# Kernel optimization log

Hardware: AMD Instinct MI355X
Metric: run time of the kernel (lower is better)

## Reference

```python
import jax, jax.numpy as jnp
import numpy as np

LN_EPS = 1e-5  # torch LayerNorm default
EPS = 1e-8     # slot-attention eps

def _ln(x, g, b):
    m = jnp.mean(x, axis=-1, keepdims=True)
    v = jnp.mean(jnp.square(x - m), axis=-1, keepdims=True)
    return (x - m) * jax.lax.rsqrt(v + LN_EPS) * g + b

def setup_inputs() -> dict:
    key = jax.random.key(0)
    ks = jax.random.split(key, 16)
    b, d, n_s, h = 131072, 256, 16, 256
    w_scale = d ** -0.5
    return {
        "inputs": jax.random.normal(ks[0], (b, 1, d), jnp.float32),
        "noise": jax.random.normal(ks[1], (n_s, d), jnp.float32),
        "slots_mu": jax.random.normal(ks[2], (1, d), jnp.float32),
        "slots_sigma": jax.random.uniform(ks[3], (1, d), jnp.float32),
        "Wq": jax.random.normal(ks[4], (d, d), jnp.float32) * w_scale,
        "bq": jnp.zeros((d,), jnp.float32),
        "Wk": jax.random.normal(ks[5], (d, d), jnp.float32) * w_scale,
        "bk": jnp.zeros((d,), jnp.float32),
        "Wv": jax.random.normal(ks[6], (d, d), jnp.float32) * w_scale,
        "bv": jnp.zeros((d,), jnp.float32),
        "W_ih": jax.random.normal(ks[7], (3 * d, d), jnp.float32) * w_scale,
        "W_hh": jax.random.normal(ks[8], (3 * d, d), jnp.float32) * w_scale,
        "b_ih": jnp.zeros((3 * d,), jnp.float32),
        "b_hh": jnp.zeros((3 * d,), jnp.float32),
        "W1": jax.random.normal(ks[9], (h, d), jnp.float32) * w_scale,
        "b1": jnp.zeros((h,), jnp.float32),
        "W2": jax.random.normal(ks[10], (d, h), jnp.float32) * (h ** -0.5),
        "b2": jnp.zeros((d,), jnp.float32),
        "g_in": jnp.ones((d,), jnp.float32),
        "be_in": jnp.zeros((d,), jnp.float32),
        "g_s": jnp.ones((d,), jnp.float32),
        "be_s": jnp.zeros((d,), jnp.float32),
        "g_f": jnp.ones((d,), jnp.float32),
        "be_f": jnp.zeros((d,), jnp.float32),
    }

def reference(inputs, noise, slots_mu, slots_sigma, Wq, bq, Wk, bk, Wv, bv,
              W_ih, W_hh, b_ih, b_hh, W1, b1, W2, b2,
              g_in, be_in, g_s, be_s, g_f, be_f):
    b, w, d = inputs.shape  # w == 1 required by the module's LayerNorm(dim)
    x = inputs.reshape(b, w * d)
    scale = d ** -0.5
    iters = 3

    slots = slots_mu + slots_sigma * noise  # (n_s, d), reparameterized normal

    x = _ln(x, g_in, be_in)
    k = x @ Wk.T + bk  # (b, d)
    v = x @ Wv.T + bv  # (b, d)

    for _ in range(iters):
        slots_prev = slots
        s = _ln(slots, g_s, be_s)
        q = s @ Wq.T + bq                      # (n_s, d)
        dots = jnp.einsum('nd,bd->nb', q, k) * scale
        attn = jax.nn.softmax(dots, axis=0) + EPS   # softmax over slots
        attn = attn / jnp.sum(attn, axis=-1, keepdims=True)
        updates = jnp.einsum('bd,nb->nd', v, attn)  # (n_s, d)
        # torch GRUCell
        gx = updates @ W_ih.T + b_ih                # (n_s, 3d)
        gh = slots_prev @ W_hh.T + b_hh
        xr, xz, xn = jnp.split(gx, 3, axis=-1)
        hr, hz, hn = jnp.split(gh, 3, axis=-1)
        r = jax.nn.sigmoid(xr + hr)
        z = jax.nn.sigmoid(xz + hz)
        n = jnp.tanh(xn + r * hn)
        slots = (1.0 - z) * n + z * slots_prev
        ff = jax.nn.relu(_ln(slots, g_f, be_f) @ W1.T + b1) @ W2.T + b2
        slots = slots + ff
    return slots
```

## Files before the change

kernel.cpp:

```cpp
#include <hip/hip_runtime.h>
#include <stdint.h>

#define B_ROWS 131072
#define SCALE 0.0625f
#define LN_EPS 1e-5f
#define ATTN_EPS 1e-8f

#define BIG_BLOCKS 512
#define BIG_THREADS 512
#define ROWS_PER_BLOCK (B_ROWS / BIG_BLOCKS)
#define ROWS_PER_WAVE  (ROWS_PER_BLOCK / 8)
#define NSLICE 8

#define WS_PARTU 0
#define WS_PARTS (WS_PARTU + 512*4096)
#define WS_U     (WS_PARTS + 512*16)
#define WS_S     (WS_U + 4096)
#define WS_SLOTS (WS_S + 64)
#define WS_MID   (WS_SLOTS + 4096)
#define WS_GX    (WS_MID + 4096)
#define WS_GH    (WS_GX + 12288)
#define WS_H1    (WS_GH + 12288)
#define WS_QKG   (WS_H1 + 4096)
#define WS_QB    (WS_QKG + 4096)
#define WS_WIHV  (WS_QB + 64)
#define WS_BGX   (WS_WIHV + 196608)
#define WS_WQKG  (WS_BGX + 768)
#define WS_U2G   (WS_WQKG + 65536)
#define WS_U1    (WS_U2G + 256)
#define WS_C1    (WS_U1 + 256)

__device__ __forceinline__ float dot16(const float* __restrict__ w, const float* s)
{
  float4 w0 = *(const float4*)(w);
  float4 w1 = *(const float4*)(w + 4);
  float4 w2 = *(const float4*)(w + 8);
  float4 w3 = *(const float4*)(w + 12);
  float4 s0 = *(const float4*)(s);
  float4 s1 = *(const float4*)(s + 4);
  float4 s2 = *(const float4*)(s + 8);
  float4 s3 = *(const float4*)(s + 12);
  float a = 0.f;
  a = fmaf(w0.x, s0.x, a); a = fmaf(w0.y, s0.y, a);
  a = fmaf(w0.z, s0.z, a); a = fmaf(w0.w, s0.w, a);
  a = fmaf(w1.x, s1.x, a); a = fmaf(w1.y, s1.y, a);
  a = fmaf(w1.z, s1.z, a); a = fmaf(w1.w, s1.w, a);
  a = fmaf(w2.x, s2.x, a); a = fmaf(w2.y, s2.y, a);
  a = fmaf(w2.z, s2.z, a); a = fmaf(w2.w, s2.w, a);
  a = fmaf(w3.x, s3.x, a); a = fmaf(w3.y, s3.y, a);
  a = fmaf(w3.z, s3.z, a); a = fmaf(w3.w, s3.w, a);
  return a;
}

__global__ __launch_bounds__(256) void k_pre1(
    const float* __restrict__ Wq, const float* __restrict__ bq,
    const float* __restrict__ Wk, const float* __restrict__ bk,
    const float* __restrict__ Wv, const float* __restrict__ bv,
    const float* __restrict__ W_ih, const float* __restrict__ b_ih,
    const float* __restrict__ g_in, const float* __restrict__ be_in,
    float* __restrict__ ws)
{
  int bid = blockIdx.x, t = threadIdx.x;
  int wave = t >> 6, lane = t & 63;
  if (bid < 32) {
#pragma unroll
    for (int q = 0; q < 4; q++)
      ws[WS_PARTU + bid * 1024 + q * 256 + t] = 0.f;
  } else if (bid == 256) {
    if (t < 128) ws[WS_PARTS + t] = 0.f;
  }
  if (bid < 192) {
    __shared__ __align__(16) float sW[4 * 256];
    __shared__ __align__(16) float sBv[256];
    int j0 = bid * 4;
#pragma unroll
    for (int r = 0; r < 4; r++) sW[r * 256 + t] = W_ih[(j0 + r) * 256 + t];
    sBv[t] = bv[t];
    __syncthreads();
    int d = t;
    float a0 = 0.f, a1 = 0.f, a2 = 0.f, a3 = 0.f;
#pragma unroll 8
    for (int dd = 0; dd < 256; dd++) {
      float v = Wv[dd * 256 + d];
      a0 = fmaf(sW[0 * 256 + dd], v, a0);
      a1 = fmaf(sW[1 * 256 + dd], v, a1);
      a2 = fmaf(sW[2 * 256 + dd], v, a2);
      a3 = fmaf(sW[3 * 256 + dd], v, a3);
    }
    ws[WS_WIHV + (j0 + 0) * 256 + d] = a0;
    ws[WS_WIHV + (j0 + 1) * 256 + d] = a1;
    ws[WS_WIHV + (j0 + 2) * 256 + d] = a2;
    ws[WS_WIHV + (j0 + 3) * 256 + d] = a3;
    float s = 0.f;
#pragma unroll
    for (int q = 0; q < 4; q++) {
      int idx = lane * 4 + q;
      s = fmaf(sW[wave * 256 + idx], sBv[idx], s);
    }
#pragma unroll
    for (int m = 1; m <= 32; m <<= 1) s += __shfl_xor(s, m);
    if (lane == 0) ws[WS_BGX + j0 + wave] = b_ih[j0 + wave] + s;
  } else if (bid < 256) {
    __shared__ __align__(16) float sKc[4 * 256];
    __shared__ __align__(16) float sBq[256];
    int c0 = (bid - 192) * 4;
#pragma unroll
    for (int r = 0; r < 4; r++) sKc[r * 256 + t] = Wk[t * 256 + c0 + r];
    sBq[t] = bq[t];
    __syncthreads();
    int d = t;
    float a0 = 0.f, a1 = 0.f, a2 = 0.f, a3 = 0.f;
#pragma unroll 8
    for (int i = 0; i < 256; i++) {
      float wq = Wq[i * 256 + d];
      a0 = fmaf(wq, sKc[0 * 256 + i], a0);
      a1 = fmaf(wq, sKc[1 * 256 + i], a1);
      a2 = fmaf(wq, sKc[2 * 256 + i], a2);
      a3 = fmaf(wq, sKc[3 * 256 + i], a3);
    }
    ws[WS_WQKG + (c0 + 0) * 256 + d] = SCALE * g_in[c0 + 0] * a0;
    ws[WS_WQKG + (c0 + 1) * 256 + d] = SCALE * g_in[c0 + 1] * a1;
    ws[WS_WQKG + (c0 + 2) * 256 + d] = SCALE * g_in[c0 + 2] * a2;
    ws[WS_WQKG + (c0 + 3) * 256 + d] = SCALE * g_in[c0 + 3] * a3;
    float s = 0.f;
#pragma unroll
    for (int q = 0; q < 4; q++) {
      int idx = lane * 4 + q;
      s = fmaf(sBq[idx], sKc[wave * 256 + idx], s);
    }
#pragma unroll
    for (int m = 1; m <= 32; m <<= 1) s += __shfl_xor(s, m);
    if (lane == 0) ws[WS_U2G + c0 + wave] = SCALE * g_in[c0 + wave] * s;
  } else {
    __shared__ __align__(16) float sBe[256];
    __shared__ __align__(16) float sT2[256];
    sBe[t] = be_in[t];
    __syncthreads();
    float a = 0.f;
#pragma unroll 8
    for (int dp = 0; dp < 256; dp += 4) {
      float4 w = *(const float4*)(Wk + t * 256 + dp);
      a = fmaf(w.x, sBe[dp], fmaf(w.y, sBe[dp + 1],
          fmaf(w.z, sBe[dp + 2], fmaf(w.w, sBe[dp + 3], a))));
    }
    sT2[t] = a + bk[t];
    __syncthreads();
    float u = 0.f;
#pragma unroll 8
    for (int i = 0; i < 256; i++)
      u = fmaf(Wq[i * 256 + t], sT2[i], u);
    ws[WS_U1 + t] = u;
    if (wave == 0) {
      float s = 0.f;
#pragma unroll
      for (int q = 0; q < 4; q++) {
        int idx = lane * 4 + q;
        s = fmaf(bq[idx], sT2[idx], s);
      }
#pragma unroll
      for (int m = 1; m <= 32; m <<= 1) s += __shfl_xor(s, m);
      if (lane == 0) ws[WS_C1] = s;
    }
  }
}

__global__ __launch_bounds__(256) void k_qkg(
    const float* __restrict__ noise, const float* __restrict__ mu,
    const float* __restrict__ sigma, const float* __restrict__ g_s,
    const float* __restrict__ be_s, float* __restrict__ ws, int init)
{
  __shared__ __align__(16) float sS[16 * 260];
  __shared__ __align__(16) float sAux[512];
  __shared__ __align__(16) float sStat[32];
  int bid = blockIdx.x, t = threadIdx.x;
  for (int n = 0; n < 16; n++) {
    float v;
    if (init) v = fmaf(sigma[t], noise[n * 256 + t], mu[t]);
    else      v = ws[WS_SLOTS + n * 256 + t];
    sS[n * 260 + t] = v;
    if (init && bid == 0) ws[WS_SLOTS + n * 256 + t] = v;
  }
  __syncthreads();
  { int n = t >> 4, c = t & 15;
    float s1 = 0.f, s2 = 0.f;
    for (int k = 0; k < 16; k++) {
      float x = sS[n * 260 + c * 16 + k];
      s1 += x; s2 = fmaf(x, x, s2);
    }
    sAux[n * 16 + c] = s1; sAux[256 + n * 16 + c] = s2; }
  __syncthreads();
  if (t < 16) {
    float s1 = 0.f, s2 = 0.f;
    for (int c = 0; c < 16; c++) { s1 += sAux[t * 16 + c]; s2 += sAux[256 + t * 16 + c]; }
    float m = s1 * (1.f / 256.f);
    float v = fmaxf(fmaf(-m, m, s2 * (1.f / 256.f)), 0.f);
    sStat[t] = m; sStat[16 + t] = rsqrtf(v + LN_EPS);
  }
  __syncthreads();
  { float gs = g_s[t], bs = be_s[t];
    for (int n = 0; n < 16; n++) {
      float m = sStat[n], rs = sStat[16 + n];
      sS[n * 260 + t] = fmaf((sS[n * 260 + t] - m) * rs, gs, bs);
    } }
  __syncthreads();
  if (bid < 64) {
    int cr = t >> 6, n = (t >> 2) & 15, ks = t & 3;
    int c = bid * 4 + cr;
    const float* wrow = ws + WS_WQKG + c * 256 + ks * 64;
    const float* srow = &sS[n * 260 + ks * 64];
    float acc = 0.f;
#pragma unroll
    for (int i = 0; i < 16; i++) {
      float4 w = *(const float4*)(wrow + i * 4);
      float4 s4 = *(const float4*)(srow + i * 4);
      acc = fmaf(w.x, s4.x, fmaf(w.y, s4.y, fmaf(w.z, s4.z, fmaf(w.w, s4.w, acc))));
    }
    sAux[t] = acc;
    __syncthreads();
    if (t < 64) {
      int cr2 = t >> 4, n2 = t & 15;
      int c2 = bid * 4 + cr2;
      int b = cr2 * 64 + n2 * 4;
      float s = sAux[b] + sAux[b + 1] + sAux[b + 2] + sAux[b + 3];
      ws[WS_QKG + n2 * 256 + c2] = s + ws[WS_U2G + c2];
    }
  } else {
    int n = t >> 4, ks = t & 15;
    float acc = 0.f;
    for (int k = 0; k < 16; k++)
      acc = fmaf(sS[n * 260 + ks * 16 + k], ws[WS_U1 + ks * 16 + k], acc);
    sAux[t] = acc;
    __syncthreads();
    if (t < 16) {
      float s = 0.f;
      for (int k = 0; k < 16; k++) s += sAux[t * 16 + k];
      ws[WS_QB + t] = SCALE * (s + ws[WS_C1]);
    }
  }
}

__global__ __launch_bounds__(512, 2) void k_big(
    const float* __restrict__ X, float* __restrict__ ws)
{
  __shared__ __align__(16) float red[4 * 4096];
  __shared__ __align__(16) float redS[128];
  int t = threadIdx.x;
  int wave = t >> 6, lane = t & 63;
  int p = lane >> 4, g = lane & 15;

  const float* qkg = ws + WS_QKG;
  float qw[4][16];
  float qs[4];
#pragma unroll
  for (int i = 0; i < 4; i++) {
    const float* rp = qkg + (4 * p + i) * 256 + g * 16;
#pragma unroll
    for (int jq = 0; jq < 4; jq++) {
      float4 v4 = *(const float4*)(rp + 4 * jq);
      qw[i][4 * jq + 0] = v4.x; qw[i][4 * jq + 1] = v4.y;
      qw[i][4 * jq + 2] = v4.z; qw[i][4 * jq + 3] = v4.w;
    }
    float s = 0.f;
#pragma unroll
    for (int j = 0; j < 16; j++) s += qw[i][j];
    qs[i] = s;
  }
#pragma unroll
  for (int m = 1; m <= 8; m <<= 1) {
#pragma unroll
    for (int i = 0; i < 4; i++) qs[i] += __shfl_xor(qs[i], m);
  }
  float qb0[4];
  {
    float4 q4 = *(const float4*)(ws + WS_QB + 4 * p);
    qb0[0] = q4.x; qb0[1] = q4.y; qb0[2] = q4.z; qb0[3] = q4.w;
  }

  float P[4][16];
#pragma unroll
  for (int i = 0; i < 4; i++)
#pragma unroll
    for (int j = 0; j < 16; j++) P[i][j] = 0.f;
  float Q[4] = {0.f, 0.f, 0.f, 0.f};
  float Sa[4] = {0.f, 0.f, 0.f, 0.f};

  size_t rowbase = (size_t)blockIdx.x * ROWS_PER_BLOCK + (size_t)wave * ROWS_PER_WAVE;
  const float* base = X + rowbase * 256 + g * 16;

  float4 cA0 = *(const float4*)(base + 0);
  float4 cB0 = *(const float4*)(base + 4);
  float4 cC0 = *(const float4*)(base + 8);
  float4 cD0 = *(const float4*)(base + 12);
  float4 cA1 = *(const float4*)(base + 256);
  float4 cB1 = *(const float4*)(base + 260);
  float4 cC1 = *(const float4*)(base + 264);
  float4 cD1 = *(const float4*)(base + 268);

#pragma unroll 1
  for (int r = 0; r < ROWS_PER_WAVE; r += 2) {
    const float* nx = base + (size_t)((r + 2 < ROWS_PER_WAVE) ? (r + 2) : 0) * 256;
    float4 pA0 = *(const float4*)(nx + 0);
    float4 pB0 = *(const float4*)(nx + 4);
    float4 pC0 = *(const float4*)(nx + 8);
    float4 pD0 = *(const float4*)(nx + 12);
    float4 pA1 = *(const float4*)(nx + 256);
    float4 pB1 = *(const float4*)(nx + 260);
    float4 pC1 = *(const float4*)(nx + 264);
    float4 pD1 = *(const float4*)(nx + 268);

    float x0[16], x1[16];
    x0[0] = cA0.x; x0[1] = cA0.y; x0[2] = cA0.z; x0[3] = cA0.w;
    x0[4] = cB0.x; x0[5] = cB0.y; x0[6] = cB0.z; x0[7] = cB0.w;
    x0[8] = cC0.x; x0[9] = cC0.y; x0[10] = cC0.z; x0[11] = cC0.w;
    x0[12] = cD0.x; x0[13] = cD0.y; x0[14] = cD0.z; x0[15] = cD0.w;
    x1[0] = cA1.x; x1[1] = cA1.y; x1[2] = cA1.z; x1[3] = cA1.w;
    x1[4] = cB1.x; x1[5] = cB1.y; x1[6] = cB1.z; x1[7] = cB1.w;
    x1[8] = cC1.x; x1[9] = cC1.y; x1[10] = cC1.z; x1[11] = cC1.w;
    x1[12] = cD1.x; x1[13] = cD1.y; x1[14] = cD1.z; x1[15] = cD1.w;

    float s10 = 0.f, s20 = 0.f, s11 = 0.f, s21 = 0.f;
    float d0[4] = {0.f, 0.f, 0.f, 0.f};
    float d1[4] = {0.f, 0.f, 0.f, 0.f};
#pragma unroll
    for (int j = 0; j < 16; j++) {
      s10 += x0[j]; s20 = fmaf(x0[j], x0[j], s20);
      s11 += x1[j]; s21 = fmaf(x1[j], x1[j], s21);
#pragma unroll
      for (int i = 0; i < 4; i++) {
        d0[i] = fmaf(qw[i][j], x0[j], d0[i]);
        d1[i] = fmaf(qw[i][j], x1[j], d1[i]);
      }
    }
#pragma unroll
    for (int m = 1; m <= 8; m <<= 1) {
      s10 += __shfl_xor(s10, m); s11 += __shfl_xor(s11, m);
      s20 += __shfl_xor(s20, m); s21 += __shfl_xor(s21, m);
#pragma unroll
      for (int i = 0; i < 4; i++) {
        d0[i] += __shfl_xor(d0[i], m);
        d1[i] += __shfl_xor(d1[i], m);
      }
    }
    float mean0 = s10 * (1.f / 256.f), mean1 = s11 * (1.f / 256.f);
    float var0 = fmaxf(fmaf(-mean0, mean0, s20 * (1.f / 256.f)), 0.f);
    float var1 = fmaxf(fmaf(-mean1, mean1, s21 * (1.f / 256.f)), 0.f);
    float rs0 = rsqrtf(var0 + LN_EPS), rs1 = rsqrtf(var1 + LN_EPS);
    float mrs0 = mean0 * rs0, mrs1 = mean1 * rs1;

    float dsc0[4], dsc1[4];
#pragma unroll
    for (int i = 0; i < 4; i++) {
      dsc0[i] = fmaf(rs0, d0[i], fmaf(-mrs0, qs[i], qb0[i]));
      dsc1[i] = fmaf(rs1, d1[i], fmaf(-mrs1, qs[i], qb0[i]));
    }

    float mx0 = fmaxf(fmaxf(dsc0[0], dsc0[1]), fmaxf(dsc0[2], dsc0[3]));
    float mx1 = fmaxf(fmaxf(dsc1[0], dsc1[1]), fmaxf(dsc1[2], dsc1[3]));
    mx0 = fmaxf(mx0, __shfl_xor(mx0, 16)); mx1 = fmaxf(mx1, __shfl_xor(mx1, 16));
    mx0 = fmaxf(mx0, __shfl_xor(mx0, 32)); mx1 = fmaxf(mx1, __shfl_xor(mx1, 32));
    float e0[4], e1[4];
#pragma unroll
    for (int i = 0; i < 4; i++) {
      e0[i] = __expf(dsc0[i] - mx0);
      e1[i] = __expf(dsc1[i] - mx1);
    }
    float se0 = e0[0] + e0[1] + e0[2] + e0[3];
    float se1 = e1[0] + e1[1] + e1[2] + e1[3];
    se0 += __shfl_xor(se0, 16); se1 += __shfl_xor(se1, 16);
    se0 += __shfl_xor(se0, 32); se1 += __shfl_xor(se1, 32);
    float inv0 = 1.0f / se0, inv1 = 1.0f / se1;
    float a0v[4], ar0[4], a1v[4], ar1[4];
#pragma unroll
    for (int i = 0; i < 4; i++) {
      a0v[i] = fmaf(e0[i], inv0, ATTN_EPS); ar0[i] = a0v[i] * rs0;
      a1v[i] = fmaf(e1[i], inv1, ATTN_EPS); ar1[i] = a1v[i] * rs1;
    }

#pragma unroll
    for (int j = 0; j < 16; j++) {
#pragma unroll
      for (int i = 0; i < 4; i++) {
        P[i][j] = fmaf(ar0[i], x0[j], P[i][j]);
        P[i][j] = fmaf(ar1[i], x1[j], P[i][j]);
      }
    }
#pragma unroll
    for (int i = 0; i < 4; i++) {
      Q[i] = fmaf(a0v[i], mrs0, Q[i]);
      Q[i] = fmaf(a1v[i], mrs1, Q[i]);
      Sa[i] += a0v[i];
      Sa[i] += a1v[i];
    }

    cA0 = pA0; cB0 = pB0; cC0 = pC0; cD0 = pD0;
    cA1 = pA1; cB1 = pB1; cC1 = pC1; cD1 = pD1;
  }

  int slot = wave & 3;
  if (wave < 4) {
#pragma unroll
    for (int i = 0; i < 4; i++) {
#pragma unroll
      for (int jq = 0; jq < 4; jq++) {
        float4 v4;
        v4.x = P[i][4 * jq + 0] - Q[i]; v4.y = P[i][4 * jq + 1] - Q[i];
        v4.z = P[i][4 * jq + 2] - Q[i]; v4.w = P[i][4 * jq + 3] - Q[i];
        *(float4*)&red[slot * 4096 + (4 * p + i) * 256 + g * 16 + jq * 4] = v4;
      }
    }
  }
  if (g == 0) {
#pragma unroll
    for (int i = 0; i < 4; i++) redS[wave * 16 + 4 * p + i] = Sa[i];
  }
  __syncthreads();
  if (wave >= 4) {
#pragma unroll
    for (int i = 0; i < 4; i++) {
#pragma unroll
      for (int jq = 0; jq < 4; jq++) {
        float4* dst = (float4*)&red[slot * 4096 + (4 * p + i) * 256 + g * 16 + jq * 4];
        float4 c = *dst;
        c.x += P[i][4 * jq + 0] - Q[i]; c.y += P[i][4 * jq + 1] - Q[i];
        c.z += P[i][4 * jq + 2] - Q[i]; c.w += P[i][4 * jq + 3] - Q[i];
        *dst = c;
      }
    }
  }
  __syncthreads();
  int slice = blockIdx.x & 7;
#pragma unroll
  for (int k = 0; k < 8; k++) {
    int idx = k * 512 + t;
    float v = red[idx] + red[4096 + idx] + red[8192 + idx] + red[12288 + idx];
    atomicAdd(&ws[WS_PARTU + (size_t)slice * 4096 + idx], v);
  }
  if (t < 16) {
    float sv = 0.f;
#pragma unroll
    for (int w = 0; w < 8; w++) sv += redS[w * 16 + t];
    atomicAdd(&ws[WS_PARTS + slice * 16 + t], sv);
  }
}

__global__ __launch_bounds__(256) void k_gxgh(
    const float* __restrict__ W_hh, const float* __restrict__ b_hh,
    const float* __restrict__ g_in, const float* __restrict__ be_in,
    float* __restrict__ ws)
{
  __shared__ __align__(16) float sU[16 * 260];
  __shared__ __align__(16) float sInv[16];
  int bid = blockIdx.x, t = threadIdx.x;
  bool isgx = bid < 64;
  if (isgx && t < 16) {
    float s = 0.f;
#pragma unroll
    for (int sl = 0; sl < NSLICE; sl++) s += ws[WS_PARTS + sl * 16 + t];
    sInv[t] = 1.0f / s;
  }
  __syncthreads();
  if (isgx) {
    float gi = g_in[t], bi = be_in[t];
    for (int n = 0; n < 16; n++) {
      float acc = 0.f;
#pragma unroll
      for (int sl = 0; sl < NSLICE; sl++)
        acc += ws[WS_PARTU + (size_t)sl * 4096 + n * 256 + t];
      sU[n * 260 + t] = fmaf(gi * acc, sInv[n], bi);
    }
  } else {
    for (int n = 0; n < 16; n++)
      sU[n * 260 + t] = ws[WS_SLOTS + n * 256 + t];
  }
  __syncthreads();
  int jr = t >> 4, n = t & 15;
  if (jr < 12) {
    int j = (isgx ? bid : bid - 64) * 12 + jr;
    const float* srow = &sU[n * 260];
    const float* wrow = isgx ? (ws + WS_WIHV + j * 256) : (W_hh + j * 256);
    float acc = isgx ? ws[WS_BGX + j] : b_hh[j];
#pragma unroll 8
    for (int k = 0; k < 64; k++) {
      float4 w = *(const float4*)(wrow + k * 4);
      float4 s4 = *(const float4*)(srow + k * 4);
      acc = fmaf(w.x, s4.x, fmaf(w.y, s4.y, fmaf(w.z, s4.z, fmaf(w.w, s4.w, acc))));
    }
    if (isgx) ws[WS_GX + n * 768 + j] = acc;
    else      ws[WS_GH + n * 768 + j] = acc;
  }
}

__global__ __launch_bounds__(512) void k_tail(
    const float* __restrict__ W1, const float* __restrict__ b1,
    const float* __restrict__ g_f, const float* __restrict__ be_f,
    const float* __restrict__ W2, const float* __restrict__ b2v,
    const float* __restrict__ g_s, const float* __restrict__ be_s,
    float* __restrict__ out, float* __restrict__ ws, int last)
{
  __shared__ __align__(16) float sMid[256];
  __shared__ __align__(16) float sVec[256];
  __shared__ __align__(16) float sH1[256];
  __shared__ __align__(16) float sNew[256];
  __shared__ __align__(16) float sR[32];
  int n = blockIdx.x, t = threadIdx.x;
  int wv = t >> 6, lane = t & 63;
  int j16 = t >> 4, kt = t & 15;

  {
    int gid = n * 512 + t;
    float4 z4 = {0.f, 0.f, 0.f, 0.f};
    *(float4*)&ws[WS_PARTU + gid * 4] = z4;
    if (n == 0 && t < 128) ws[WS_PARTS + t] = 0.f;
  }

  float mid = 0.f;
  if (t < 256) {
    float xr = ws[WS_GX + n * 768 + t],       hr = ws[WS_GH + n * 768 + t];
    float xz = ws[WS_GX + n * 768 + 256 + t], hz = ws[WS_GH + n * 768 + 256 + t];
    float xn = ws[WS_GX + n * 768 + 512 + t], hn = ws[WS_GH + n * 768 + 512 + t];
    float sp = ws[WS_SLOTS + n * 256 + t];
    float r = 1.f / (1.f + __expf(-(xr + hr)));
    float z = 1.f / (1.f + __expf(-(xz + hz)));
    float nn = tanhf(fmaf(r, hn, xn));
    mid = fmaf(z, sp - nn, nn);
    sMid[t] = mid;
  }

  {
    float s1 = mid, s2 = mid * mid;
#pragma unroll
    for (int m = 1; m <= 32; m <<= 1) {
      s1 += __shfl_xor(s1, m); s2 += __shfl_xor(s2, m);
    }
    if (lane == 0) { sR[wv] = s1; sR[8 + wv] = s2; }
  }
  __syncthreads();
  {
    float s1 = sR[0] + sR[1] + sR[2] + sR[3] + sR[4] + sR[5] + sR[6] + sR[7];
    float s2 = sR[8] + sR[9] + sR[10] + sR[11] + sR[12] + sR[13] + sR[14] + sR[15];
    float mean = s1 * (1.f / 256.f);
    float var = fmaxf(fmaf(-mean, mean, s2 * (1.f / 256.f)), 0.f);
    float rs = rsqrtf(var + LN_EPS);
    if (t < 256)
      sVec[t] = fmaf((sMid[t] - mean) * rs, g_f[t], be_f[t]);
  }
  __syncthreads();

#pragma unroll 2
  for (int pass = 0; pass < 8; pass++) {
    int j = pass * 32 + j16;
    float a = dot16(W1 + (size_t)j * 256 + kt * 16, sVec + kt * 16);
    a += __shfl_xor(a, 1); a += __shfl_xor(a, 2);
    a += __shfl_xor(a, 4); a += __shfl_xor(a, 8);
    if (kt == 0) sH1[j] = fmaxf(a + b1[j], 0.f);
  }
  __syncthreads();

#pragma unroll 2
  for (int pass = 0; pass < 8; pass++) {
    int d = pass * 32 + j16;
    float a = dot16(W2 + (size_t)d * 256 + kt * 16, sH1 + kt * 16);
    a += __shfl_xor(a, 1); a += __shfl_xor(a, 2);
    a += __shfl_xor(a, 4); a += __shfl_xor(a, 8);
    if (kt == 0) sNew[d] = a + b2v[d] + sMid[d];
  }
  __syncthreads();
  if (t < 256) {
    float v = sNew[t];
    ws[WS_SLOTS + n * 256 + t] = v;
    out[n * 256 + t] = v;
  }
  if (last) return;

  {
    float v = (t < 256) ? sNew[t] : 0.f;
    float s1 = v, s2 = v * v;
#pragma unroll
    for (int m = 1; m <= 32; m <<= 1) {
      s1 += __shfl_xor(s1, m); s2 += __shfl_xor(s2, m);
    }
    if (lane == 0) { sR[wv] = s1; sR[8 + wv] = s2; }
  }
  __syncthreads();
  {
    float s1 = sR[0] + sR[1] + sR[2] + sR[3] + sR[4] + sR[5] + sR[6] + sR[7];
    float s2 = sR[8] + sR[9] + sR[10] + sR[11] + sR[12] + sR[13] + sR[14] + sR[15];
    float mean = s1 * (1.f / 256.f);
    float var = fmaxf(fmaf(-mean, mean, s2 * (1.f / 256.f)), 0.f);
    float rs = rsqrtf(var + LN_EPS);
    if (t < 256)
      sVec[t] = fmaf((sNew[t] - mean) * rs, g_s[t], be_s[t]);
  }
  __syncthreads();
#pragma unroll 2
  for (int pass = 0; pass < 8; pass++) {
    int c = pass * 32 + j16;
    float a = dot16(ws + WS_WQKG + (size_t)c * 256 + kt * 16, sVec + kt * 16);
    a += __shfl_xor(a, 1); a += __shfl_xor(a, 2);
    a += __shfl_xor(a, 4); a += __shfl_xor(a, 8);
    if (kt == 0) ws[WS_QKG + n * 256 + c] = a + ws[WS_U2G + c];
  }
  {
    float pq = (t < 256) ? sVec[t] * ws[WS_U1 + t] : 0.f;
#pragma unroll
    for (int m = 1; m <= 32; m <<= 1) pq += __shfl_xor(pq, m);
    if (lane == 0) sR[wv] = pq;
  }
  __syncthreads();
  if (t == 0) {
    float s = sR[0] + sR[1] + sR[2] + sR[3] + sR[4] + sR[5] + sR[6] + sR[7];
    ws[WS_QB + n] = SCALE * (s + ws[WS_C1]);
  }
}

extern "C" void kernel_launch(void* const* d_in, const int* in_sizes, int n_in,
                              void* d_out, int out_size, void* d_ws, size_t ws_size,
                              hipStream_t stream)
{
  (void)in_sizes; (void)n_in; (void)out_size; (void)ws_size;
  const float* inputs = (const float*)d_in[0];
  const float* noise  = (const float*)d_in[1];
  const float* mu     = (const float*)d_in[2];
  const float* sigma  = (const float*)d_in[3];
  const float* Wq     = (const float*)d_in[4];
  const float* bq     = (const float*)d_in[5];
  const float* Wk     = (const float*)d_in[6];
  const float* bk     = (const float*)d_in[7];
  const float* Wv     = (const float*)d_in[8];
  const float* bv     = (const float*)d_in[9];
  const float* W_ih   = (const float*)d_in[10];
  const float* W_hh   = (const float*)d_in[11];
  const float* b_ih   = (const float*)d_in[12];
  const float* b_hh   = (const float*)d_in[13];
  const float* W1     = (const float*)d_in[14];
  const float* b1     = (const float*)d_in[15];
  const float* W2     = (const float*)d_in[16];
  const float* b2     = (const float*)d_in[17];
  const float* g_in   = (const float*)d_in[18];
  const float* be_in  = (const float*)d_in[19];
  const float* g_s    = (const float*)d_in[20];
  const float* be_s   = (const float*)d_in[21];
  const float* g_f    = (const float*)d_in[22];
  const float* be_f   = (const float*)d_in[23];
  float* ws = (float*)d_ws;
  float* out = (float*)d_out;

  hipLaunchKernelGGL(k_pre1, dim3(257), dim3(256), 0, stream,
                     Wq, bq, Wk, bk, Wv, bv, W_ih, b_ih, g_in, be_in, ws);
  hipLaunchKernelGGL(k_qkg, dim3(65), dim3(256), 0, stream,
                     noise, mu, sigma, g_s, be_s, ws, 1);
  for (int it = 0; it < 3; it++) {
    hipLaunchKernelGGL(k_big, dim3(BIG_BLOCKS), dim3(BIG_THREADS), 0, stream,
                       inputs, ws);
    hipLaunchKernelGGL(k_gxgh, dim3(128), dim3(256), 0, stream,
                       W_hh, b_hh, g_in, be_in, ws);
    hipLaunchKernelGGL(k_tail, dim3(16), dim3(512), 0, stream,
                       W1, b1, g_f, be_f, W2, b2, g_s, be_s,
                       out, ws, (it == 2) ? 1 : 0);
  }
}
```

Before: 549.0 us.

## Fuse GRU gate and tail kernels via software grid barrier

Merges the gx/gh gate kernel and the slot tail kernel into one 128-block launch that uses an atomic-counter grid barrier, after which 16 blocks run the GRU/MLP tail with 256 threads instead of 512. This removes one kernel launch and its inter-kernel gap per iteration, which matters because the small kernels are latency-bound. The cost is a spin barrier that assumes all 128 blocks are co-resident, and half as many threads in the tail matvecs.

```diff
diff --git a/kernel.cpp b/kernel.cpp
--- a/kernel.cpp
+++ b/kernel.cpp
@@ -11,6 +11,7 @@
 #define ROWS_PER_BLOCK (B_ROWS / BIG_BLOCKS)
 #define ROWS_PER_WAVE  (ROWS_PER_BLOCK / 8)
 #define NSLICE 8
+#define SLOT_BLOCKS 128u
 
 #define WS_PARTU 0
 #define WS_PARTS (WS_PARTU + 512*4096)
@@ -29,6 +30,21 @@
 #define WS_U2G   (WS_WQKG + 65536)
 #define WS_U1    (WS_U2G + 256)
 #define WS_C1    (WS_U1 + 256)
+#define WS_CTR   (WS_C1 + 4)
+
+__device__ __forceinline__ void gridbar(unsigned int* ctr, unsigned int target)
+{
+  __syncthreads();
+  if (threadIdx.x == 0) {
+    __threadfence();
+    __hip_atomic_fetch_add(ctr, 1u, __ATOMIC_RELEASE, __HIP_MEMORY_SCOPE_AGENT);
+    while (__hip_atomic_load(ctr, __ATOMIC_RELAXED, __HIP_MEMORY_SCOPE_AGENT) < target) {
+      __builtin_amdgcn_s_sleep(1);
+    }
+    __threadfence();
+  }
+  __syncthreads();
+}
 
 __device__ __forceinline__ float dot16(const float* __restrict__ w, const float* s)
 {
@@ -68,6 +84,7 @@
       ws[WS_PARTU + bid * 1024 + q * 256 + t] = 0.f;
   } else if (bid == 256) {
     if (t < 128) ws[WS_PARTS + t] = 0.f;
+    if (t == 0) *((unsigned int*)(ws + WS_CTR)) = 0u;
   }
   if (bid < 192) {
     __shared__ __align__(16) float sW[4 * 256];
@@ -443,78 +460,81 @@
   }
 }
 
-__global__ __launch_bounds__(256) void k_gxgh(
+__global__ __launch_bounds__(256) void k_slot(
     const float* __restrict__ W_hh, const float* __restrict__ b_hh,
     const float* __restrict__ g_in, const float* __restrict__ be_in,
-    float* __restrict__ ws)
-{
-  __shared__ __align__(16) float sU[16 * 260];
-  __shared__ __align__(16) float sInv[16];
-  int bid = blockIdx.x, t = threadIdx.x;
-  bool isgx = bid < 64;
-  if (isgx && t < 16) {
-    float s = 0.f;
-#pragma unroll
-    for (int sl = 0; sl < NSLICE; sl++) s += ws[WS_PARTS + sl * 16 + t];
-    sInv[t] = 1.0f / s;
-  }
-  __syncthreads();
-  if (isgx) {
-    float gi = g_in[t], bi = be_in[t];
-    for (int n = 0; n < 16; n++) {
-      float acc = 0.f;
-#pragma unroll
-      for (int sl = 0; sl < NSLICE; sl++)
-        acc += ws[WS_PARTU + (size_t)sl * 4096 + n * 256 + t];
-      sU[n * 260 + t] = fmaf(gi * acc, sInv[n], bi);
-    }
-  } else {
-    for (int n = 0; n < 16; n++)
-      sU[n * 260 + t] = ws[WS_SLOTS + n * 256 + t];
-  }
-  __syncthreads();
-  int jr = t >> 4, n = t & 15;
-  if (jr < 12) {
-    int j = (isgx ? bid : bid - 64) * 12 + jr;
-    const float* srow = &sU[n * 260];
-    const float* wrow = isgx ? (ws + WS_WIHV + j * 256) : (W_hh + j * 256);
-    float acc = isgx ? ws[WS_BGX + j] : b_hh[j];
-#pragma unroll 8
-    for (int k = 0; k < 64; k++) {
-      float4 w = *(const float4*)(wrow + k * 4);
-      float4 s4 = *(const float4*)(srow + k * 4);
-      acc = fmaf(w.x, s4.x, fmaf(w.y, s4.y, fmaf(w.z, s4.z, fmaf(w.w, s4.w, acc))));
-    }
-    if (isgx) ws[WS_GX + n * 768 + j] = acc;
-    else      ws[WS_GH + n * 768 + j] = acc;
-  }
-}
-
-__global__ __launch_bounds__(512) void k_tail(
     const float* __restrict__ W1, const float* __restrict__ b1,
     const float* __restrict__ g_f, const float* __restrict__ be_f,
     const float* __restrict__ W2, const float* __restrict__ b2v,
     const float* __restrict__ g_s, const float* __restrict__ be_s,
-    float* __restrict__ out, float* __restrict__ ws, int last)
+    float* __restrict__ out, float* __restrict__ ws, int it, int last)
 {
-  __shared__ __align__(16) float sMid[256];
-  __shared__ __align__(16) float sVec[256];
-  __shared__ __align__(16) float sH1[256];
-  __shared__ __align__(16) float sNew[256];
-  __shared__ __align__(16) float sR[32];
-  int n = blockIdx.x, t = threadIdx.x;
+  __shared__ __align__(16) float sU[16 * 260];
+  __shared__ __align__(16) float sInv[16];
+  __shared__ __align__(16) float sR[16];
+  int bid = blockIdx.x, t = threadIdx.x;
   int wv = t >> 6, lane = t & 63;
+  unsigned int* ctr = (unsigned int*)(ws + WS_CTR);
+
+  {
+    bool isgx = bid < 64;
+    if (isgx && t < 16) {
+      float s = 0.f;
+#pragma unroll
+      for (int sl = 0; sl < NSLICE; sl++) s += ws[WS_PARTS + sl * 16 + t];
+      sInv[t] = 1.0f / s;
+    }
+    __syncthreads();
+    if (isgx) {
+      float gi = g_in[t], bi = be_in[t];
+      for (int n = 0; n < 16; n++) {
+        float acc = 0.f;
+#pragma unroll
+        for (int sl = 0; sl < NSLICE; sl++)
+          acc += ws[WS_PARTU + (size_t)sl * 4096 + n * 256 + t];
+        sU[n * 260 + t] = fmaf(gi * acc, sInv[n], bi);
+      }
+    } else {
+      for (int n = 0; n < 16; n++)
+        sU[n * 260 + t] = ws[WS_SLOTS + n * 256 + t];
+    }
+    __syncthreads();
+    int jr = t >> 4, n = t & 15;
+    if (jr < 12) {
+      int j = (isgx ? bid : bid - 64) * 12 + jr;
+      const float* srow = &sU[n * 260];
+      const float* wrow = isgx ? (ws + WS_WIHV + j * 256) : (W_hh + j * 256);
+      float acc = isgx ? ws[WS_BGX + j] : b_hh[j];
+#pragma unroll 8
+      for (int k = 0; k < 64; k++) {
+        float4 w = *(const float4*)(wrow + k * 4);
+        float4 s4 = *(const float4*)(srow + k * 4);
+        acc = fmaf(w.x, s4.x, fmaf(w.y, s4.y, fmaf(w.z, s4.z, fmaf(w.w, s4.w, acc))));
+      }
+      if (isgx) ws[WS_GX + n * 768 + j] = acc;
+      else      ws[WS_GH + n * 768 + j] = acc;
+    }
+  }
+
+  gridbar(ctr, (unsigned int)(it + 1) * SLOT_BLOCKS);
+  if (bid >= 16) return;
+
+  float* sMid = sU;
+  float* sVec = sU + 260;
+  float* sH1  = sU + 520;
+  float* sNew = sU + 780;
+  int n = bid;
   int j16 = t >> 4, kt = t & 15;
 
   {
-    int gid = n * 512 + t;
     float4 z4 = {0.f, 0.f, 0.f, 0.f};
-    *(float4*)&ws[WS_PARTU + gid * 4] = z4;
+    *(float4*)&ws[WS_PARTU + (n * 512 + t) * 4] = z4;
+    *(float4*)&ws[WS_PARTU + (n * 512 + 256 + t) * 4] = z4;
     if (n == 0 && t < 128) ws[WS_PARTS + t] = 0.f;
   }
 
-  float mid = 0.f;
-  if (t < 256) {
+  float mid;
+  {
     float xr = ws[WS_GX + n * 768 + t],       hr = ws[WS_GH + n * 768 + t];
     float xz = ws[WS_GX + n * 768 + 256 + t], hz = ws[WS_GH + n * 768 + 256 + t];
     float xn = ws[WS_GX + n * 768 + 512 + t], hn = ws[WS_GH + n * 768 + 512 + t];
@@ -525,7 +545,6 @@
     mid = fmaf(z, sp - nn, nn);
     sMid[t] = mid;
   }
-
   {
     float s1 = mid, s2 = mid * mid;
 #pragma unroll
@@ -536,36 +555,33 @@
   }
   __syncthreads();
   {
-    float s1 = sR[0] + sR[1] + sR[2] + sR[3] + sR[4] + sR[5] + sR[6] + sR[7];
-    float s2 = sR[8] + sR[9] + sR[10] + sR[11] + sR[12] + sR[13] + sR[14] + sR[15];
+    float s1 = sR[0] + sR[1] + sR[2] + sR[3];
+    float s2 = sR[8] + sR[9] + sR[10] + sR[11];
     float mean = s1 * (1.f / 256.f);
     float var = fmaxf(fmaf(-mean, mean, s2 * (1.f / 256.f)), 0.f);
     float rs = rsqrtf(var + LN_EPS);
-    if (t < 256)
-      sVec[t] = fmaf((sMid[t] - mean) * rs, g_f[t], be_f[t]);
-  }
-  __syncthreads();
-
+    sVec[t] = fmaf((sMid[t] - mean) * rs, g_f[t], be_f[t]);
+  }
+  __syncthreads();
 #pragma unroll 2
-  for (int pass = 0; pass < 8; pass++) {
-    int j = pass * 32 + j16;
+  for (int pass = 0; pass < 16; pass++) {
+    int j = pass * 16 + j16;
     float a = dot16(W1 + (size_t)j * 256 + kt * 16, sVec + kt * 16);
     a += __shfl_xor(a, 1); a += __shfl_xor(a, 2);
     a += __shfl_xor(a, 4); a += __shfl_xor(a, 8);
     if (kt == 0) sH1[j] = fmaxf(a + b1[j], 0.f);
   }
   __syncthreads();
-
 #pragma unroll 2
-  for (int pass = 0; pass < 8; pass++) {
-    int d = pass * 32 + j16;
+  for (int pass = 0; pass < 16; pass++) {
+    int d = pass * 16 + j16;
     float a = dot16(W2 + (size_t)d * 256 + kt * 16, sH1 + kt * 16);
     a += __shfl_xor(a, 1); a += __shfl_xor(a, 2);
     a += __shfl_xor(a, 4); a += __shfl_xor(a, 8);
     if (kt == 0) sNew[d] = a + b2v[d] + sMid[d];
   }
   __syncthreads();
-  if (t < 256) {
+  {
     float v = sNew[t];
     ws[WS_SLOTS + n * 256 + t] = v;
     out[n * 256 + t] = v;
@@ -573,7 +589,7 @@
   if (last) return;
 
   {
-    float v = (t < 256) ? sNew[t] : 0.f;
+    float v = sNew[t];
     float s1 = v, s2 = v * v;
 #pragma unroll
     for (int m = 1; m <= 32; m <<= 1) {
@@ -583,32 +599,31 @@
   }
   __syncthreads();
   {
-    float s1 = sR[0] + sR[1] + sR[2] + sR[3] + sR[4] + sR[5] + sR[6] + sR[7];
-    float s2 = sR[8] + sR[9] + sR[10] + sR[11] + sR[12] + sR[13] + sR[14] + sR[15];
+    float s1 = sR[0] + sR[1] + sR[2] + sR[3];
+    float s2 = sR[8] + sR[9] + sR[10] + sR[11];
     float mean = s1 * (1.f / 256.f);
     float var = fmaxf(fmaf(-mean, mean, s2 * (1.f / 256.f)), 0.f);
     float rs = rsqrtf(var + LN_EPS);
-    if (t < 256)
-      sVec[t] = fmaf((sNew[t] - mean) * rs, g_s[t], be_s[t]);
+    sVec[t] = fmaf((sNew[t] - mean) * rs, g_s[t], be_s[t]);
   }
   __syncthreads();
 #pragma unroll 2
-  for (int pass = 0; pass < 8; pass++) {
-    int c = pass * 32 + j16;
+  for (int pass = 0; pass < 16; pass++) {
+    int c = pass * 16 + j16;
     float a = dot16(ws + WS_WQKG + (size_t)c * 256 + kt * 16, sVec + kt * 16);
     a += __shfl_xor(a, 1); a += __shfl_xor(a, 2);
     a += __shfl_xor(a, 4); a += __shfl_xor(a, 8);
     if (kt == 0) ws[WS_QKG + n * 256 + c] = a + ws[WS_U2G + c];
   }
   {
-    float pq = (t < 256) ? sVec[t] * ws[WS_U1 + t] : 0.f;
+    float pq = sVec[t] * ws[WS_U1 + t];
 #pragma unroll
     for (int m = 1; m <= 32; m <<= 1) pq += __shfl_xor(pq, m);
     if (lane == 0) sR[wv] = pq;
   }
   __syncthreads();
   if (t == 0) {
-    float s = sR[0] + sR[1] + sR[2] + sR[3] + sR[4] + sR[5] + sR[6] + sR[7];
+    float s = sR[0] + sR[1] + sR[2] + sR[3];
     ws[WS_QB + n] = SCALE * (s + ws[WS_C1]);
   }
 }
@@ -652,10 +667,8 @@
   for (int it = 0; it < 3; it++) {
     hipLaunchKernelGGL(k_big, dim3(BIG_BLOCKS), dim3(BIG_THREADS), 0, stream,
                        inputs, ws);
-    hipLaunchKernelGGL(k_gxgh, dim3(128), dim3(256), 0, stream,
-                       W_hh, b_hh, g_in, be_in, ws);
-    hipLaunchKernelGGL(k_tail, dim3(16), dim3(512), 0, stream,
-                       W1, b1, g_f, be_f, W2, b2, g_s, be_s,
-                       out, ws, (it == 2) ? 1 : 0);
+    hipLaunchKernelGGL(k_slot, dim3(SLOT_BLOCKS), dim3(256), 0, stream,
+                       W_hh, b_hh, g_in, be_in, W1, b1, g_f, be_f,
+                       W2, b2, g_s, be_s, out, ws, it, (it == 2) ? 1 : 0);
   }
 }
```

After: 613.9 us. 1.12x slower.
